# Kernel tuning notes

Measured on AMD Instinct MI355X. Metric: run time of the kernel, lower is better.

The kernel has to match this reference:

```python
import jax, jax.numpy as jnp
import numpy as np

N = 50000          # nodes (num_sensors)
E = 600000         # edges
IN_DIM = 75        # 3 * 25
DIMS = [(75, 128), (128, 128), (128, 32)]  # (in, out) per layer: in->hidden->hidden->bottleneck


def setup_inputs() -> dict:
    key = jax.random.key(0)
    ks = jax.random.split(key, 4 + 5 * len(DIMS))
    inp = {
        "x": jax.random.normal(ks[0], (N, IN_DIM), dtype=jnp.float32),
        "edge_index": jax.random.randint(ks[1], (2, E), 0, N, dtype=jnp.int64),
        "weight": jax.random.uniform(ks[2], (E,), dtype=jnp.float32),
        "sim": jax.random.normal(ks[3], (E, 2), dtype=jnp.float32),
    }
    i = 4
    for l, (cin, cout) in enumerate(DIMS):
        s = jnp.float32(1.0 / np.sqrt(cin))
        inp[f"wr{l}"] = jax.random.normal(ks[i + 0], (cin, cout), dtype=jnp.float32) * s  # real part of complex conv filter
        inp[f"wi{l}"] = jax.random.normal(ks[i + 1], (cin, cout), dtype=jnp.float32) * s  # imag part
        inp[f"cb{l}"] = jnp.zeros((cout,), dtype=jnp.float32)                              # conv bias
        inp[f"lw{l}"] = jax.random.normal(ks[i + 2], (cout, cin), dtype=jnp.float32) * s  # Linear weight (torch layout [out,in])
        inp[f"lb{l}"] = jnp.zeros((cout,), dtype=jnp.float32)                              # Linear bias
        i += 5
    return inp


def _layer(x, src, dst, cr, ci, wr, wi, cb, lw, lb):
    # ModeConvFast: gather source features, scale by complex edge coefficient
    # c = weight * (sim_r + i*sim_i), scatter-add to destination nodes,
    # project with complex filter W = wr + i*wi, keep real part, add bias.
    xs = x[src]                                   # [E, Cin] gather
    agg_r = jax.ops.segment_sum(xs * cr[:, None], dst, num_segments=N)  # [N, Cin]
    agg_i = jax.ops.segment_sum(xs * ci[:, None], dst, num_segments=N)  # [N, Cin]
    conv = agg_r @ wr - agg_i @ wi + cb           # real part of complex matmul
    return jax.nn.relu(conv + x @ lw.T + lb)      # conv(x,...) + lin(x), then relu


def reference(x, edge_index, weight, sim,
              wr0, wi0, cb0, lw0, lb0,
              wr1, wi1, cb1, lw1, lb1,
              wr2, wi2, cb2, lw2, lb2):
    src, dst = edge_index[0], edge_index[1]
    cr = weight * sim[:, 0]                       # [E] real edge coefficient
    ci = weight * sim[:, 1]                       # [E] imag edge coefficient
    layers = [
        (wr0, wi0, cb0, lw0, lb0),
        (wr1, wi1, cb1, lw1, lb1),
        (wr2, wi2, cb2, lw2, lb2),
    ]
    for p in layers:
        x = _layer(x, src, dst, cr, ci, *p)
    return x
```

## Files before the change

### kernel.cpp

```cpp
#include <hip/hip_runtime.h>

#define N_NODES 50000
#define N_EDGES 600000
#define E_PAD_MAX (N_EDGES + N_NODES * 7)

using bf16x8 = __attribute__((ext_vector_type(8))) short;
using f32x4  = __attribute__((ext_vector_type(4))) float;
typedef unsigned int uint32_tt;

__device__ __forceinline__ unsigned short f2bf(float f) {
    union { float f; unsigned int u; } v; v.f = f;
    unsigned int u = v.u;
    return (unsigned short)((u + 0x7fffu + ((u >> 16) & 1u)) >> 16);
}
__device__ __forceinline__ float bf2f(unsigned int h16) {
    union { unsigned int u; float f; } v; v.u = h16 << 16;
    return v.f;
}


__global__ void hist_kernel(const int* __restrict__ ei, int* __restrict__ cnt, int E) {
    int e = blockIdx.x * 256 + threadIdx.x;
    if (e < E) atomicAdd(&cnt[ei[E + e]], 1);
}

__global__ void scan1(const int* __restrict__ deg, int* __restrict__ out,
                      int* __restrict__ bsum, int n) {
    __shared__ int s[256];
    int t = threadIdx.x;
    int base = blockIdx.x * 1024 + t * 4;
    int v0 = (base + 0 < n) ? ((deg[base + 0] + 7) & ~7) : 0;
    int v1 = (base + 1 < n) ? ((deg[base + 1] + 7) & ~7) : 0;
    int v2 = (base + 2 < n) ? ((deg[base + 2] + 7) & ~7) : 0;
    int v3 = (base + 3 < n) ? ((deg[base + 3] + 7) & ~7) : 0;
    int tsum = v0 + v1 + v2 + v3;
    s[t] = tsum;
    __syncthreads();
    for (int off = 1; off < 256; off <<= 1) {
        int tmp = (t >= off) ? s[t - off] : 0;
        __syncthreads();
        s[t] += tmp;
        __syncthreads();
    }
    int excl = s[t] - tsum;
    if (base + 0 < n) out[base + 0] = excl;
    if (base + 1 < n) out[base + 1] = excl + v0;
    if (base + 2 < n) out[base + 2] = excl + v0 + v1;
    if (base + 3 < n) out[base + 3] = excl + v0 + v1 + v2;
    if (t == 255) bsum[blockIdx.x] = s[255];
}

__global__ void scan2(int* __restrict__ bsum, int nb) {
    if (threadIdx.x == 0 && blockIdx.x == 0) {
        int acc = 0;
        for (int i = 0; i < nb; ++i) { int v = bsum[i]; bsum[i] = acc; acc += v; }
        bsum[nb] = acc;
    }
}

__global__ void scan3(int* __restrict__ off, const int* __restrict__ bsum,
                      int* __restrict__ cnt, int n, int nb) {
    int i = blockIdx.x * 256 + threadIdx.x;
    if (i < n) { off[i] += bsum[i >> 10]; cnt[i] = 0; }
    if (i == n) off[n] = bsum[nb];
}

__global__ void scatter_kernel(const int* __restrict__ ei, const float* __restrict__ w,
                               const float* __restrict__ sim, const int* __restrict__ off,
                               int* __restrict__ cnt, uint2* __restrict__ edat, int E) {
    int e = blockIdx.x * 256 + threadIdx.x;
    if (e >= E) return;
    int s = ei[e], d = ei[E + e];
    int p = off[d] + atomicAdd(&cnt[d], 1);
    float wt = w[e];
    uint2 m;
    m.x = (unsigned)s;
    m.y = (uint32_tt)f2bf(wt * sim[2 * e]) |
          ((uint32_tt)f2bf(wt * sim[2 * e + 1]) << 16);
    edat[p] = m;
}

__global__ void prep_kernel(
    const float* __restrict__ x0, unsigned short* __restrict__ xb,
    const float* __restrict__ wr0, const float* __restrict__ wi0,
    const float* __restrict__ lw0, unsigned short* __restrict__ BT0,
    const float* __restrict__ wr1, const float* __restrict__ wi1,
    const float* __restrict__ lw1, unsigned short* __restrict__ BT1,
    const float* __restrict__ wr2, const float* __restrict__ wi2,
    const float* __restrict__ lw2, unsigned short* __restrict__ BT2, int n) {
    int i = blockIdx.x * 256 + threadIdx.x;
    int nconv = n * 96;
    if (i < nconv) {
        int r = i / 96, c = i - r * 96;
        xb[i] = (c < 75) ? f2bf(x0[r * 75 + c]) : (unsigned short)0;
        return;
    }
    i -= nconv;
    if (i < 128 * 288) {
        int nn = i / 288, k = i - nn * 288;
        int part = k / 96, kk = k - part * 96;
        float v = 0.f;
        if (kk < 75) {
            if (part == 0)      v = wr0[kk * 128 + nn];
            else if (part == 1) v = -wi0[kk * 128 + nn];
            else                v = lw0[nn * 75 + kk];
        }
        BT0[i] = f2bf(v);
        return;
    }
    i -= 128 * 288;
    if (i < 128 * 384) {
        int nn = i / 384, k = i - nn * 384;
        int part = k >> 7, kk = k & 127;
        float v;
        if (part == 0)      v = wr1[kk * 128 + nn];
        else if (part == 1) v = -wi1[kk * 128 + nn];
        else                v = lw1[nn * 128 + kk];
        BT1[i] = f2bf(v);
        return;
    }
    i -= 128 * 384;
    if (i < 96 * 128) {
        int nn = i >> 7, k = i & 127;
        float v;
        if (nn < 32)      v = wr2[k * 32 + nn];
        else if (nn < 64) v = -wi2[k * 32 + (nn - 32)];
        else              v = lw2[(nn - 64) * 128 + k];
        BT2[i] = f2bf(v);
    }
}

template <int CU2>
__global__ __launch_bounds__(256) void agg_bf16(
    const uint32_tt* __restrict__ x, const int* __restrict__ off,
    const uint2* __restrict__ edat, uint32_tt* __restrict__ aggR,
    uint32_tt* __restrict__ aggI, int n) {
    int wave = threadIdx.x >> 6;
    int lane = threadIdx.x & 63;
    int node = __builtin_amdgcn_readfirstlane(blockIdx.x * 4 + wave);
    if (node >= n) return;
    int lc = (CU2 == 64) ? lane : (lane < CU2 ? lane : CU2 - 1);
    float arl = 0.f, arh = 0.f, ail = 0.f, aih = 0.f;
    int e0 = __builtin_amdgcn_readfirstlane(off[node]);
    int e1 = __builtin_amdgcn_readfirstlane(off[node + 1]);

    if (e0 < e1) {
        uint2 m[8];
#pragma unroll
        for (int j = 0; j < 8; ++j) m[j] = edat[e0 + j];
        for (int e = e0; e < e1; e += 8) {
            int sj[8]; float crj[8], cij[8];
#pragma unroll
            for (int j = 0; j < 8; ++j) {
                sj[j] = __builtin_amdgcn_readfirstlane((int)m[j].x);
                int pk = __builtin_amdgcn_readfirstlane((int)m[j].y);
                crj[j] = bf2f((unsigned)pk & 0xffffu);
                cij[j] = bf2f((unsigned)pk >> 16);
            }
            uint32_tt w[8];
#pragma unroll
            for (int j = 0; j < 8; ++j) {
                const uint32_tt* rowp = x + (size_t)sj[j] * CU2;
                w[j] = rowp[lc];
            }
            if (e + 8 < e1) {
#pragma unroll
                for (int j = 0; j < 8; ++j) m[j] = edat[e + 8 + j];
            }
#pragma unroll
            for (int j = 0; j < 8; ++j) {
                float lo = bf2f(w[j] & 0xffffu), hi = bf2f(w[j] >> 16);
                arl += crj[j] * lo; arh += crj[j] * hi;
                ail += cij[j] * lo; aih += cij[j] * hi;
            }
        }
    }
    if (lane < CU2) {
        aggR[(size_t)node * CU2 + lane] = (uint32_tt)f2bf(arl) | ((uint32_tt)f2bf(arh) << 16);
        aggI[(size_t)node * CU2 + lane] = (uint32_tt)f2bf(ail) | ((uint32_tt)f2bf(aih) << 16);
    }
}

__global__ __launch_bounds__(256) void agg_out(
    const uint32_tt* __restrict__ Y, const int* __restrict__ off,
    const uint2* __restrict__ edat, const float* __restrict__ cb,
    const float* __restrict__ lb, float* __restrict__ out, int n) {
    int wave = threadIdx.x >> 6;
    int lane = threadIdx.x & 63;
    int node = __builtin_amdgcn_readfirstlane(blockIdx.x * 4 + wave);
    if (node >= n) return;
    int lc = (lane < 32) ? lane : 31;
    int usei = (lane >> 4) & 1;
    float alo = 0.f, ahi = 0.f;
    int e0 = __builtin_amdgcn_readfirstlane(off[node]);
    int e1 = __builtin_amdgcn_readfirstlane(off[node + 1]);

    if (e0 < e1) {
        uint2 m[8];
#pragma unroll
        for (int j = 0; j < 8; ++j) m[j] = edat[e0 + j];
        for (int e = e0; e < e1; e += 8) {
            int sj[8]; float crj[8], cij[8];
#pragma unroll
            for (int j = 0; j < 8; ++j) {
                sj[j] = __builtin_amdgcn_readfirstlane((int)m[j].x);
                int pk = __builtin_amdgcn_readfirstlane((int)m[j].y);
                crj[j] = bf2f((unsigned)pk & 0xffffu);
                cij[j] = bf2f((unsigned)pk >> 16);
            }
            uint32_tt w[8];
#pragma unroll
            for (int j = 0; j < 8; ++j) {
                const uint32_tt* rowp = Y + (size_t)sj[j] * 48;
                w[j] = rowp[lc];
            }
            if (e + 8 < e1) {
#pragma unroll
                for (int j = 0; j < 8; ++j) m[j] = edat[e + 8 + j];
            }
#pragma unroll
            for (int j = 0; j < 8; ++j) {
                float c = usei ? cij[j] : crj[j];
                float lo = bf2f(w[j] & 0xffffu), hi = bf2f(w[j] >> 16);
                alo += c * lo; ahi += c * hi;
            }
        }
    }
    alo += __shfl_xor(alo, 16);
    ahi += __shfl_xor(ahi, 16);
    if (lane < 16) {
        uint32_tt lin = Y[(size_t)node * 48 + 32 + lane];
        int c0 = 2 * lane, c1 = 2 * lane + 1;
        float v0 = alo + bf2f(lin & 0xffffu) + cb[c0] + lb[c0];
        float v1 = ahi + bf2f(lin >> 16) + cb[c1] + lb[c1];
        float2 r;
        r.x = v0 > 0.f ? v0 : 0.f;
        r.y = v1 > 0.f ? v1 : 0.f;
        ((float2*)out)[(size_t)node * 16 + lane] = r;
    }
}

template <int CINP, int COUT, int BM, int WM, int WN, int MT, int NT,
          bool OUT_BF16, bool RAW, int PARTS>
__global__ __launch_bounds__(256) void gemm_mfma(
    const unsigned short* __restrict__ A0, const unsigned short* __restrict__ A1,
    const unsigned short* __restrict__ A2, const unsigned short* __restrict__ BT,
    const float* __restrict__ cb, const float* __restrict__ lb,
    void* __restrict__ outv, int n) {
    constexpr int PK = 40;
    constexpr int KTOT = PARTS * CINP;
    constexpr int NCH = KTOT / 32;
    constexpr int CPP = CINP / 32;
    __shared__ unsigned short sA[BM][PK];
    __shared__ unsigned short sB[COUT][PK];

    int t = threadIdx.x;
    int lane = t & 63, wave = t >> 6;
    int wm = wave / WN, wn = wave % WN;
    int ml = lane & 15, kh = lane >> 4;
    int node0 = blockIdx.x * BM;

    const unsigned short* Asrc[3] = {A0, A1, A2};

    f32x4 acc[MT][NT];
#pragma unroll
    for (int mt = 0; mt < MT; ++mt)
#pragma unroll
        for (int nt = 0; nt < NT; ++nt) acc[mt][nt] = (f32x4){0.f, 0.f, 0.f, 0.f};

    for (int c = 0; c < NCH; ++c) {
        int part = (PARTS == 1) ? 0 : (c / CPP);
        int kk = (c - part * CPP) * 32;
        const unsigned short* __restrict__ Ap = Asrc[part];
        __syncthreads();
#pragma unroll
        for (int i = t; i < BM * 4; i += 256) {
            int r = i >> 2, q = i & 3;
            int node = node0 + r;
            if (node >= n) node = n - 1;
            *(uint4*)&sA[r][q * 8] =
                *(const uint4*)(Ap + (size_t)node * CINP + kk + q * 8);
        }
#pragma unroll
        for (int i = t; i < COUT * 4; i += 256) {
            int r = i >> 2, q = i & 3;
            *(uint4*)&sB[r][q * 8] =
                *(const uint4*)(BT + (size_t)r * KTOT + c * 32 + q * 8);
        }
        __syncthreads();
        bf16x8 af[MT], bfr[NT];
#pragma unroll
        for (int mt = 0; mt < MT; ++mt)
            af[mt] = *(const bf16x8*)&sA[wm * (MT * 16) + mt * 16 + ml][kh * 8];
#pragma unroll
        for (int nt = 0; nt < NT; ++nt)
            bfr[nt] = *(const bf16x8*)&sB[wn * (NT * 16) + nt * 16 + ml][kh * 8];
#pragma unroll
        for (int mt = 0; mt < MT; ++mt)
#pragma unroll
            for (int nt = 0; nt < NT; ++nt)
                acc[mt][nt] = __builtin_amdgcn_mfma_f32_16x16x32_bf16(
                    af[mt], bfr[nt], acc[mt][nt], 0, 0, 0);
    }

    int row0 = kh * 4;
#pragma unroll
    for (int nt = 0; nt < NT; ++nt) {
        int col = wn * (NT * 16) + nt * 16 + ml;
        float bias = RAW ? 0.f : (cb[col] + lb[col]);
#pragma unroll
        for (int mt = 0; mt < MT; ++mt) {
#pragma unroll
            for (int r = 0; r < 4; ++r) {
                int node = node0 + wm * (MT * 16) + mt * 16 + row0 + r;
                if (node < n) {
                    float v = acc[mt][nt][r] + bias;
                    if (!RAW) v = v > 0.f ? v : 0.f;
                    if (OUT_BF16)
                        ((unsigned short*)outv)[(size_t)node * COUT + col] = f2bf(v);
                    else
                        ((float*)outv)[(size_t)node * COUT + col] = v;
                }
            }
        }
    }
}


extern "C" void kernel_launch(void* const* d_in, const int* in_sizes, int n_in,
                              void* d_out, int out_size, void* d_ws, size_t ws_size,
                              hipStream_t stream) {
    const float* x0  = (const float*)d_in[0];
    const int*   ei  = (const int*)d_in[1];
    const float* wgt = (const float*)d_in[2];
    const float* sim = (const float*)d_in[3];
    const float *wr[3], *wi[3], *cb[3], *lw[3], *lb[3];
    for (int l = 0; l < 3; ++l) {
        wr[l] = (const float*)d_in[4 + 5 * l];
        wi[l] = (const float*)d_in[5 + 5 * l];
        cb[l] = (const float*)d_in[6 + 5 * l];
        lw[l] = (const float*)d_in[7 + 5 * l];
        lb[l] = (const float*)d_in[8 + 5 * l];
    }

    char* p = (char*)d_ws;
    auto alloc = [&](size_t bytes) -> void* {
        void* r = p;
        p += (bytes + 255) & ~(size_t)255;
        return r;
    };
    int*   off  = (int*)alloc((N_NODES + 1) * 4);
    int*   cnt  = (int*)alloc(N_NODES * 4);
    int*   bsum = (int*)alloc(256);
    uint2* edat = (uint2*)alloc((size_t)E_PAD_MAX * 8);
    unsigned short* xb    = (unsigned short*)alloc((size_t)N_NODES * 96 * 2);
    unsigned short* aggRb = (unsigned short*)alloc((size_t)N_NODES * 128 * 2);
    unsigned short* aggIb = (unsigned short*)alloc((size_t)N_NODES * 128 * 2);
    unsigned short* h1b   = (unsigned short*)alloc((size_t)N_NODES * 128 * 2);
    unsigned short* h2b   = (unsigned short*)alloc((size_t)N_NODES * 128 * 2);
    unsigned short* Yb    = (unsigned short*)alloc((size_t)N_NODES * 96 * 2);
    unsigned short* BT0   = (unsigned short*)alloc((size_t)128 * 288 * 2);
    unsigned short* BT1   = (unsigned short*)alloc((size_t)128 * 384 * 2);
    unsigned short* BT2   = (unsigned short*)alloc((size_t)96 * 128 * 2);
    float* outp = (float*)d_out;

    hipMemsetAsync(cnt, 0, N_NODES * 4, stream);
    hipMemsetAsync(edat, 0, (size_t)E_PAD_MAX * 8, stream);
    hist_kernel<<<(N_EDGES + 255) / 256, 256, 0, stream>>>(ei, cnt, N_EDGES);
    int nb = (N_NODES + 1023) / 1024;
    scan1<<<nb, 256, 0, stream>>>(cnt, off, bsum, N_NODES);
    scan2<<<1, 64, 0, stream>>>(bsum, nb);
    scan3<<<(N_NODES + 1 + 255) / 256, 256, 0, stream>>>(off, bsum, cnt, N_NODES, nb);
    scatter_kernel<<<(N_EDGES + 255) / 256, 256, 0, stream>>>(ei, wgt, sim, off, cnt,
                                                              edat, N_EDGES);
    {
        int total = N_NODES * 96 + 128 * 288 + 128 * 384 + 96 * 128;
        prep_kernel<<<(total + 255) / 256, 256, 0, stream>>>(
            x0, xb, wr[0], wi[0], lw[0], BT0, wr[1], wi[1], lw[1], BT1,
            wr[2], wi[2], lw[2], BT2, N_NODES);
    }

    int agrid = (N_NODES + 3) / 4;

    agg_bf16<48><<<agrid, 256, 0, stream>>>((const uint32_tt*)xb, off, edat,
                                            (uint32_tt*)aggRb, (uint32_tt*)aggIb, N_NODES);
    gemm_mfma<96, 128, 128, 2, 2, 4, 4, true, false, 3>
        <<<(N_NODES + 127) / 128, 256, 0, stream>>>(aggRb, aggIb, xb, BT0, cb[0], lb[0],
                                                    h1b, N_NODES);
    agg_bf16<64><<<agrid, 256, 0, stream>>>((const uint32_tt*)h1b, off, edat,
                                            (uint32_tt*)aggRb, (uint32_tt*)aggIb, N_NODES);
    gemm_mfma<128, 128, 128, 2, 2, 4, 4, true, false, 3>
        <<<(N_NODES + 127) / 128, 256, 0, stream>>>(aggRb, aggIb, h1b, BT1, cb[1], lb[1],
                                                    h2b, N_NODES);
    gemm_mfma<128, 96, 128, 2, 2, 4, 3, true, true, 1>
        <<<(N_NODES + 127) / 128, 256, 0, stream>>>(h2b, h2b, h2b, BT2, cb[2], lb[2],
                                                    Yb, N_NODES);
    agg_out<<<agrid, 256, 0, stream>>>((const uint32_tt*)Yb, off, edat, cb[2], lb[2],
                                       outp, N_NODES);
}
```

Measured before the change: 294.9 us.

## Fuse CSR build into one cooperative kernel and software-pipeline aggregation gathers

```diff
diff --git a/kernel.cpp b/kernel.cpp
--- a/kernel.cpp
+++ b/kernel.cpp
@@ -1,8 +1,11 @@
 #include <hip/hip_runtime.h>
+#include <hip/hip_cooperative_groups.h>
 
 #define N_NODES 50000
 #define N_EDGES 600000
 #define E_PAD_MAX (N_EDGES + N_NODES * 7)
+#define CSR_BLOCKS 512
+#define CSR_SEG ((N_NODES + CSR_BLOCKS - 1) / CSR_BLOCKS)
 
 using bf16x8 = __attribute__((ext_vector_type(8))) short;
 using f32x4  = __attribute__((ext_vector_type(4))) float;
@@ -18,66 +21,75 @@
     return v.f;
 }
 
-
-__global__ void hist_kernel(const int* __restrict__ ei, int* __restrict__ cnt, int E) {
-    int e = blockIdx.x * 256 + threadIdx.x;
-    if (e < E) atomicAdd(&cnt[ei[E + e]], 1);
-}
-
-__global__ void scan1(const int* __restrict__ deg, int* __restrict__ out,
-                      int* __restrict__ bsum, int n) {
+__global__ __launch_bounds__(256) void csr_build(
+    const int* __restrict__ ei, const float* __restrict__ wgt,
+    const float* __restrict__ sim, int* __restrict__ cnt,
+    int* __restrict__ off, int* __restrict__ bsum, uint2* __restrict__ edat) {
+    cooperative_groups::grid_group grid = cooperative_groups::this_grid();
+    int t = threadIdx.x;
+    int tid = blockIdx.x * 256 + t;
+    int nth = gridDim.x * 256;
     __shared__ int s[256];
-    int t = threadIdx.x;
-    int base = blockIdx.x * 1024 + t * 4;
-    int v0 = (base + 0 < n) ? ((deg[base + 0] + 7) & ~7) : 0;
-    int v1 = (base + 1 < n) ? ((deg[base + 1] + 7) & ~7) : 0;
-    int v2 = (base + 2 < n) ? ((deg[base + 2] + 7) & ~7) : 0;
-    int v3 = (base + 3 < n) ? ((deg[base + 3] + 7) & ~7) : 0;
-    int tsum = v0 + v1 + v2 + v3;
-    s[t] = tsum;
+
+    for (int i = tid; i < N_NODES; i += nth) cnt[i] = 0;
+    uint2 z; z.x = 0u; z.y = 0u;
+    for (int i = tid; i < E_PAD_MAX; i += nth) edat[i] = z;
+    grid.sync();
+
+    for (int e = tid; e < N_EDGES; e += nth) atomicAdd(&cnt[ei[N_EDGES + e]], 1);
+    grid.sync();
+
+    int base = blockIdx.x * CSR_SEG;
+    int v = 0;
+    bool act = (t < CSR_SEG) && (base + t < N_NODES);
+    if (act) v = (cnt[base + t] + 7) & ~7;
+    s[t] = v;
     __syncthreads();
-    for (int off = 1; off < 256; off <<= 1) {
-        int tmp = (t >= off) ? s[t - off] : 0;
+    for (int o = 1; o < 256; o <<= 1) {
+        int tmp = (t >= o) ? s[t - o] : 0;
         __syncthreads();
         s[t] += tmp;
         __syncthreads();
     }
-    int excl = s[t] - tsum;
-    if (base + 0 < n) out[base + 0] = excl;
-    if (base + 1 < n) out[base + 1] = excl + v0;
-    if (base + 2 < n) out[base + 2] = excl + v0 + v1;
-    if (base + 3 < n) out[base + 3] = excl + v0 + v1 + v2;
+    int excl = s[t] - v;
+    if (act) off[base + t] = excl;
     if (t == 255) bsum[blockIdx.x] = s[255];
-}
-
-__global__ void scan2(int* __restrict__ bsum, int nb) {
-    if (threadIdx.x == 0 && blockIdx.x == 0) {
-        int acc = 0;
-        for (int i = 0; i < nb; ++i) { int v = bsum[i]; bsum[i] = acc; acc += v; }
-        bsum[nb] = acc;
-    }
-}
-
-__global__ void scan3(int* __restrict__ off, const int* __restrict__ bsum,
-                      int* __restrict__ cnt, int n, int nb) {
-    int i = blockIdx.x * 256 + threadIdx.x;
-    if (i < n) { off[i] += bsum[i >> 10]; cnt[i] = 0; }
-    if (i == n) off[n] = bsum[nb];
-}
-
-__global__ void scatter_kernel(const int* __restrict__ ei, const float* __restrict__ w,
-                               const float* __restrict__ sim, const int* __restrict__ off,
-                               int* __restrict__ cnt, uint2* __restrict__ edat, int E) {
-    int e = blockIdx.x * 256 + threadIdx.x;
-    if (e >= E) return;
-    int s = ei[e], d = ei[E + e];
-    int p = off[d] + atomicAdd(&cnt[d], 1);
-    float wt = w[e];
-    uint2 m;
-    m.x = (unsigned)s;
-    m.y = (uint32_tt)f2bf(wt * sim[2 * e]) |
-          ((uint32_tt)f2bf(wt * sim[2 * e + 1]) << 16);
-    edat[p] = m;
+    grid.sync();
+
+    if (blockIdx.x == 0) {
+        int a = bsum[2 * t], b = bsum[2 * t + 1];
+        int pair = a + b;
+        s[t] = pair;
+        __syncthreads();
+        for (int o = 1; o < 256; o <<= 1) {
+            int tmp = (t >= o) ? s[t - o] : 0;
+            __syncthreads();
+            s[t] += tmp;
+            __syncthreads();
+        }
+        int e2 = s[t] - pair;
+        bsum[2 * t] = e2;
+        bsum[2 * t + 1] = e2 + a;
+        if (t == 255) bsum[CSR_BLOCKS] = s[255];
+    }
+    grid.sync();
+
+    int add = bsum[blockIdx.x];
+    if (act) off[base + t] += add;
+    for (int i = tid; i < N_NODES; i += nth) cnt[i] = 0;
+    if (tid == 0) off[N_NODES] = bsum[CSR_BLOCKS];
+    grid.sync();
+
+    for (int e = tid; e < N_EDGES; e += nth) {
+        int sr = ei[e], d = ei[N_EDGES + e];
+        int p = off[d] + atomicAdd(&cnt[d], 1);
+        float wt = wgt[e];
+        uint2 m;
+        m.x = (unsigned)sr;
+        m.y = (uint32_tt)f2bf(wt * sim[2 * e]) |
+              ((uint32_tt)f2bf(wt * sim[2 * e + 1]) << 16);
+        edat[p] = m;
+    }
 }
 
 __global__ void prep_kernel(
@@ -145,33 +157,53 @@
     int e1 = __builtin_amdgcn_readfirstlane(off[node + 1]);
 
     if (e0 < e1) {
-        uint2 m[8];
-#pragma unroll
-        for (int j = 0; j < 8; ++j) m[j] = edat[e0 + j];
-        for (int e = e0; e < e1; e += 8) {
-            int sj[8]; float crj[8], cij[8];
-#pragma unroll
-            for (int j = 0; j < 8; ++j) {
-                sj[j] = __builtin_amdgcn_readfirstlane((int)m[j].x);
-                int pk = __builtin_amdgcn_readfirstlane((int)m[j].y);
-                crj[j] = bf2f((unsigned)pk & 0xffffu);
-                cij[j] = bf2f((unsigned)pk >> 16);
-            }
-            uint32_tt w[8];
-#pragma unroll
-            for (int j = 0; j < 8; ++j) {
-                const uint32_tt* rowp = x + (size_t)sj[j] * CU2;
-                w[j] = rowp[lc];
-            }
-            if (e + 8 < e1) {
-#pragma unroll
-                for (int j = 0; j < 8; ++j) m[j] = edat[e + 8 + j];
-            }
-#pragma unroll
-            for (int j = 0; j < 8; ++j) {
-                float lo = bf2f(w[j] & 0xffffu), hi = bf2f(w[j] >> 16);
-                arl += crj[j] * lo; arh += crj[j] * hi;
-                ail += cij[j] * lo; aih += cij[j] * hi;
+        uint2 mn[8];
+        int sc[8]; float crc[8], cic[8];
+        uint32_tt wc[8];
+        {
+            uint2 m0[8];
+#pragma unroll
+            for (int j = 0; j < 8; ++j) m0[j] = edat[e0 + j];
+#pragma unroll
+            for (int j = 0; j < 8; ++j) {
+                sc[j] = __builtin_amdgcn_readfirstlane((int)m0[j].x);
+                int pk = __builtin_amdgcn_readfirstlane((int)m0[j].y);
+                crc[j] = bf2f((unsigned)pk & 0xffffu);
+                cic[j] = bf2f((unsigned)pk >> 16);
+            }
+            int nb = (e0 + 8 < e1) ? e0 + 8 : e0;
+#pragma unroll
+            for (int j = 0; j < 8; ++j) mn[j] = edat[nb + j];
+#pragma unroll
+            for (int j = 0; j < 8; ++j) wc[j] = x[(size_t)sc[j] * CU2 + lc];
+        }
+        for (int e = e0;; e += 8) {
+            bool more = (e + 8 < e1);
+            int sn[8]; float crn[8], cin_[8]; uint32_tt wn[8];
+            if (more) {
+#pragma unroll
+                for (int j = 0; j < 8; ++j) {
+                    sn[j] = __builtin_amdgcn_readfirstlane((int)mn[j].x);
+                    int pk = __builtin_amdgcn_readfirstlane((int)mn[j].y);
+                    crn[j] = bf2f((unsigned)pk & 0xffffu);
+                    cin_[j] = bf2f((unsigned)pk >> 16);
+                }
+                int nb = (e + 16 < e1) ? e + 16 : e + 8;
+#pragma unroll
+                for (int j = 0; j < 8; ++j) mn[j] = edat[nb + j];
+#pragma unroll
+                for (int j = 0; j < 8; ++j) wn[j] = x[(size_t)sn[j] * CU2 + lc];
+            }
+#pragma unroll
+            for (int j = 0; j < 8; ++j) {
+                float lo = bf2f(wc[j] & 0xffffu), hi = bf2f(wc[j] >> 16);
+                arl += crc[j] * lo; arh += crc[j] * hi;
+                ail += cic[j] * lo; aih += cic[j] * hi;
+            }
+            if (!more) break;
+#pragma unroll
+            for (int j = 0; j < 8; ++j) {
+                sc[j] = sn[j]; crc[j] = crn[j]; cic[j] = cin_[j]; wc[j] = wn[j];
             }
         }
     }
@@ -196,33 +228,53 @@
     int e1 = __builtin_amdgcn_readfirstlane(off[node + 1]);
 
     if (e0 < e1) {
-        uint2 m[8];
-#pragma unroll
-        for (int j = 0; j < 8; ++j) m[j] = edat[e0 + j];
-        for (int e = e0; e < e1; e += 8) {
-            int sj[8]; float crj[8], cij[8];
-#pragma unroll
-            for (int j = 0; j < 8; ++j) {
-                sj[j] = __builtin_amdgcn_readfirstlane((int)m[j].x);
-                int pk = __builtin_amdgcn_readfirstlane((int)m[j].y);
-                crj[j] = bf2f((unsigned)pk & 0xffffu);
-                cij[j] = bf2f((unsigned)pk >> 16);
-            }
-            uint32_tt w[8];
-#pragma unroll
-            for (int j = 0; j < 8; ++j) {
-                const uint32_tt* rowp = Y + (size_t)sj[j] * 48;
-                w[j] = rowp[lc];
-            }
-            if (e + 8 < e1) {
-#pragma unroll
-                for (int j = 0; j < 8; ++j) m[j] = edat[e + 8 + j];
-            }
-#pragma unroll
-            for (int j = 0; j < 8; ++j) {
-                float c = usei ? cij[j] : crj[j];
-                float lo = bf2f(w[j] & 0xffffu), hi = bf2f(w[j] >> 16);
+        uint2 mn[8];
+        int sc[8]; float crc[8], cic[8];
+        uint32_tt wc[8];
+        {
+            uint2 m0[8];
+#pragma unroll
+            for (int j = 0; j < 8; ++j) m0[j] = edat[e0 + j];
+#pragma unroll
+            for (int j = 0; j < 8; ++j) {
+                sc[j] = __builtin_amdgcn_readfirstlane((int)m0[j].x);
+                int pk = __builtin_amdgcn_readfirstlane((int)m0[j].y);
+                crc[j] = bf2f((unsigned)pk & 0xffffu);
+                cic[j] = bf2f((unsigned)pk >> 16);
+            }
+            int nb = (e0 + 8 < e1) ? e0 + 8 : e0;
+#pragma unroll
+            for (int j = 0; j < 8; ++j) mn[j] = edat[nb + j];
+#pragma unroll
+            for (int j = 0; j < 8; ++j) wc[j] = Y[(size_t)sc[j] * 48 + lc];
+        }
+        for (int e = e0;; e += 8) {
+            bool more = (e + 8 < e1);
+            int sn[8]; float crn[8], cin_[8]; uint32_tt wn[8];
+            if (more) {
+#pragma unroll
+                for (int j = 0; j < 8; ++j) {
+                    sn[j] = __builtin_amdgcn_readfirstlane((int)mn[j].x);
+                    int pk = __builtin_amdgcn_readfirstlane((int)mn[j].y);
+                    crn[j] = bf2f((unsigned)pk & 0xffffu);
+                    cin_[j] = bf2f((unsigned)pk >> 16);
+                }
+                int nb = (e + 16 < e1) ? e + 16 : e + 8;
+#pragma unroll
+                for (int j = 0; j < 8; ++j) mn[j] = edat[nb + j];
+#pragma unroll
+                for (int j = 0; j < 8; ++j) wn[j] = Y[(size_t)sn[j] * 48 + lc];
+            }
+#pragma unroll
+            for (int j = 0; j < 8; ++j) {
+                float c = usei ? cic[j] : crc[j];
+                float lo = bf2f(wc[j] & 0xffffu), hi = bf2f(wc[j] >> 16);
                 alo += c * lo; ahi += c * hi;
+            }
+            if (!more) break;
+#pragma unroll
+            for (int j = 0; j < 8; ++j) {
+                sc[j] = sn[j]; crc[j] = crn[j]; cic[j] = cin_[j]; wc[j] = wn[j];
             }
         }
     }
@@ -351,7 +403,7 @@
     };
     int*   off  = (int*)alloc((N_NODES + 1) * 4);
     int*   cnt  = (int*)alloc(N_NODES * 4);
-    int*   bsum = (int*)alloc(256);
+    int*   bsum = (int*)alloc((CSR_BLOCKS + 2) * 4);
     uint2* edat = (uint2*)alloc((size_t)E_PAD_MAX * 8);
     unsigned short* xb    = (unsigned short*)alloc((size_t)N_NODES * 96 * 2);
     unsigned short* aggRb = (unsigned short*)alloc((size_t)N_NODES * 128 * 2);
@@ -364,15 +416,14 @@
     unsigned short* BT2   = (unsigned short*)alloc((size_t)96 * 128 * 2);
     float* outp = (float*)d_out;
 
-    hipMemsetAsync(cnt, 0, N_NODES * 4, stream);
-    hipMemsetAsync(edat, 0, (size_t)E_PAD_MAX * 8, stream);
-    hist_kernel<<<(N_EDGES + 255) / 256, 256, 0, stream>>>(ei, cnt, N_EDGES);
-    int nb = (N_NODES + 1023) / 1024;
-    scan1<<<nb, 256, 0, stream>>>(cnt, off, bsum, N_NODES);
-    scan2<<<1, 64, 0, stream>>>(bsum, nb);
-    scan3<<<(N_NODES + 1 + 255) / 256, 256, 0, stream>>>(off, bsum, cnt, N_NODES, nb);
-    scatter_kernel<<<(N_EDGES + 255) / 256, 256, 0, stream>>>(ei, wgt, sim, off, cnt,
-                                                              edat, N_EDGES);
+    {
+        const int* ei_ = ei; const float* wgt_ = wgt; const float* sim_ = sim;
+        int* cnt_ = cnt; int* off_ = off; int* bsum_ = bsum; uint2* edat_ = edat;
+        void* args[] = {(void*)&ei_, (void*)&wgt_, (void*)&sim_, (void*)&cnt_,
+                        (void*)&off_, (void*)&bsum_, (void*)&edat_};
+        hipLaunchCooperativeKernel((const void*)csr_build, dim3(CSR_BLOCKS),
+                                   dim3(256), args, 0, stream);
+    }
     {
         int total = N_NODES * 96 + 128 * 288 + 128 * 384 + 96 * 128;
         prep_kernel<<<(total + 255) / 256, 256, 0, stream>>>(
```

Result: slower. 581.3 us (+97.1%).
